# Kernel tuning notes

Measured on AMD Instinct MI355X. Metric: run time of the kernel, lower is better.

Reference implementation:

```python
import jax, jax.numpy as jnp
import numpy as np

B, N, S, D, H, ITERS = 32, 4096, 24, 256, 4, 3
DH = D // H
SCALE = DH ** -0.5
EPS = 1e-8
LN_EPS = 1e-5


def _ln(x, g, b):
    m = x.mean(-1, keepdims=True)
    v = ((x - m) ** 2).mean(-1, keepdims=True)
    return (x - m) * jax.lax.rsqrt(v + LN_EPS) * g + b


def setup_inputs() -> dict:
    key = jax.random.key(0)
    ks = jax.random.split(key, 20)
    xav = lambda k, fi, fo: jax.random.uniform(k, (fi, fo), jnp.float32, -1.0, 1.0) * np.sqrt(6.0 / (fi + fo))
    u = lambda k, shp, fan: jax.random.uniform(k, shp, jnp.float32, -1.0, 1.0) / np.sqrt(fan)
    return {
        "extracted_features": jax.random.normal(ks[0], (B, N, D), jnp.float32),
        "conditioning": jax.random.normal(ks[1], (B, S, D), jnp.float32),
        "pos_ln_g": jnp.ones((D,), jnp.float32),
        "pos_ln_b": jnp.zeros((D,), jnp.float32),
        "pos_w1": xav(ks[2], D, D),
        "pos_b1": jnp.zeros((D,), jnp.float32),
        "pos_w2": xav(ks[3], D, D),
        "pos_b2": jnp.zeros((D,), jnp.float32),
        "in_ln_g": jnp.ones((D,), jnp.float32),
        "in_ln_b": jnp.zeros((D,), jnp.float32),
        "slot_ln_g": jnp.ones((D,), jnp.float32),
        "slot_ln_b": jnp.zeros((D,), jnp.float32),
        "Wq": u(ks[4], (D, D), D),
        "Wk": u(ks[5], (D, D), D),
        "Wv": u(ks[6], (D, D), D),
        "gru_wi": u(ks[7], (D, 3 * D), D),  # x @ gru_wi, torch weight_ih.T
        "gru_wh": u(ks[8], (D, 3 * D), D),
        "gru_bi": u(ks[9], (3 * D,), D),
        "gru_bh": u(ks[10], (3 * D,), D),
    }


def reference(extracted_features, conditioning, pos_ln_g, pos_ln_b, pos_w1, pos_b1,
              pos_w2, pos_b2, in_ln_g, in_ln_b, slot_ln_g, slot_ln_b,
              Wq, Wk, Wv, gru_wi, gru_wh, gru_bi, gru_bh):
    b, n, _ = extracted_features.shape
    s = conditioning.shape[1]
    # positional embedding MLP: LN -> Linear -> ReLU -> Linear
    feats = _ln(extracted_features, pos_ln_g, pos_ln_b)
    feats = jax.nn.relu(feats @ pos_w1 + pos_b1) @ pos_w2 + pos_b2
    # slot attention input norm + k/v projections
    inp = _ln(feats, in_ln_g, in_ln_b)
    k = (inp @ Wk).reshape(b, n, H, DH)
    v = (inp @ Wv).reshape(b, n, H, DH)

    slots = conditioning
    attn_before = None
    for _ in range(ITERS):
        slots_prev = slots
        sn = _ln(slots, slot_ln_g, slot_ln_b)
        q = (sn @ Wq).reshape(b, s, H, DH)
        dots = jnp.einsum('bihd,bjhd->bihj', q, k) * SCALE  # [b,s,H,n]
        # softmax over flattened (slot, head) axis per input token
        attn = jax.nn.softmax(dots.reshape(b, s * H, n), axis=1).reshape(b, s, H, n)
        attn_before = attn
        attn_r = (attn + EPS)
        attn_r = attn_r / attn_r.sum(-1, keepdims=True)
        updates = jnp.einsum('bjhd,bihj->bihd', v, attn_r).reshape(b * s, D)
        # GRUCell update
        h = slots_prev.reshape(b * s, D)
        gi = updates @ gru_wi + gru_bi
        gh = h @ gru_wh + gru_bh
        ir, iz, inn = jnp.split(gi, 3, axis=-1)
        hr, hz, hn = jnp.split(gh, 3, axis=-1)
        r = jax.nn.sigmoid(ir + hr)
        z = jax.nn.sigmoid(iz + hz)
        nn_ = jnp.tanh(inn + r * hn)
        slots = ((1.0 - z) * nn_ + z * h).reshape(b, s, D)

    return slots, attn_before.mean(axis=2)
```

## Files before the change

kernel.cpp:

```cpp
#include <hip/hip_runtime.h>
#include <hip/hip_bf16.h>
#include <stdint.h>

typedef __hip_bfloat16 bf16;
typedef __attribute__((ext_vector_type(8))) short short8;
typedef __attribute__((ext_vector_type(4))) float floatx4;

#define DEV __device__ __forceinline__

DEV float bf2f(bf16 v) { return __bfloat162float(v); }
DEV bf16 f2b(float f) { return __float2bfloat16(f); }
DEV unsigned short f2bu(float f) {
  bf16 h = __float2bfloat16(f);
  union { bf16 h; unsigned short u; } c; c.h = h; return c.u;
}
DEV bool is_bf16_in(const void* probe) { return ((const unsigned short*)probe)[0] != 0; }


__global__ __launch_bounds__(256) void params_kernel(
    const void* s0, const void* s1, const void* s2, const void* s3, const void* s4,
    const void* s5, const void* s6, const void* s7, const void* s8, const void* s9,
    float* dst)
{
  int idx = blockIdx.x * 256 + threadIdx.x;
  if (idx >= 3584) return;
  bool bf = is_bf16_in(s0);
  const void* srcs[10] = {s0, s1, s2, s3, s4, s5, s6, s7, s8, s9};
  int a, off;
  if (idx < 2048)      { a = idx >> 8; off = idx & 255; }
  else if (idx < 2816) { a = 8; off = idx - 2048; }
  else                 { a = 9; off = idx - 2816; }
  float v = bf ? bf2f(((const bf16*)srcs[a])[off]) : ((const float*)srcs[a])[off];
  dst[idx] = v;
}

__global__ __launch_bounds__(256) void transpose_all_kernel(
    const void* w1, const void* w2, const void* wq, const void* wk, const void* wv,
    const void* gwi, const void* gwh,
    bf16* d1, bf16* d2, bf16* dq, bf16* dk, bf16* dv, bf16* dgi, bf16* dgh,
    const void* probe)
{
  int idx = blockIdx.x * 256 + threadIdx.x;
  if (idx >= 720896) return;
  bool bf = is_bf16_in(probe);
  const void* src; bf16* dst; int C, off;
  if (idx < 327680) {
    int wsel = idx >> 16; off = idx & 65535; C = 256;
    const void* S[5] = {w1, w2, wq, wk, wv};
    bf16* D[5] = {d1, d2, dq, dk, dv};
    src = S[wsel]; dst = D[wsel];
  } else {
    int j = idx - 327680; int wsel = j / 196608; off = j - wsel * 196608; C = 768;
    src = wsel ? gwh : gwi; dst = wsel ? dgh : dgi;
  }
  int r = off / C, c = off - r * C;
  bf16 v = bf ? ((const bf16*)src)[off] : f2b(((const float*)src)[off]);
  dst[(size_t)c * 256 + r] = v;
}

__global__ __launch_bounds__(256) void init_slots_kernel(
    const void* __restrict__ cond, float* __restrict__ sF, bf16* __restrict__ sB,
    const void* probe)
{
  int idx = blockIdx.x * 256 + threadIdx.x;
  bool bf = is_bf16_in(probe);
  float v = bf ? bf2f(((const bf16*)cond)[idx]) : ((const float*)cond)[idx];
  sF[idx] = v;
  sB[idx] = f2b(v);
}

template<bool OUT_BF16, bool RELU, bool HAS_BIAS>
DEV void gemm_body(const bf16* __restrict__ A, const bf16* __restrict__ Bt,
                   const float* __restrict__ bias, void* __restrict__ C,
                   int M, int N, int K, int bx, int by, short* As, short* Bs)
{
  const int tid = threadIdx.x;
  const int lane = tid & 63;
  const int wave = tid >> 6;
  const int wr = wave >> 1, wc = wave & 1;
  const int m16 = lane & 15, quad = lane >> 4;
  const long m0 = (long)by * 128, n0 = (long)bx * 128;

  floatx4 acc[4][4];
#pragma unroll
  for (int i = 0; i < 4; i++)
#pragma unroll
    for (int j = 0; j < 4; j++) acc[i][j] = {0.f, 0.f, 0.f, 0.f};

  const int srow = tid >> 3;
  const int scol = (tid & 7) * 8;

  for (int kb = 0; kb < K; kb += 64) {
#pragma unroll
    for (int p = 0; p < 4; p++) {
      int row = srow + p * 32;
      uint4 av = *(const uint4*)(A + (m0 + row) * (long)K + kb + scol);
      *(uint4*)(&As[row * 72 + scol]) = av;
      uint4 bv = *(const uint4*)(Bt + (n0 + row) * (long)K + kb + scol);
      *(uint4*)(&Bs[row * 72 + scol]) = bv;
    }
    __syncthreads();
#pragma unroll
    for (int ks = 0; ks < 2; ks++) {
      short8 af[4], bfr[4];
#pragma unroll
      for (int t = 0; t < 4; t++) {
        af[t]  = *(const short8*)(&As[(wr * 64 + t * 16 + m16) * 72 + ks * 32 + quad * 8]);
        bfr[t] = *(const short8*)(&Bs[(wc * 64 + t * 16 + m16) * 72 + ks * 32 + quad * 8]);
      }
#pragma unroll
      for (int mt = 0; mt < 4; mt++)
#pragma unroll
        for (int nt = 0; nt < 4; nt++)
          acc[mt][nt] = __builtin_amdgcn_mfma_f32_16x16x32_bf16(af[mt], bfr[nt], acc[mt][nt], 0, 0, 0);
    }
    __syncthreads();
  }

#pragma unroll
  for (int mt = 0; mt < 4; mt++) {
#pragma unroll
    for (int nt = 0; nt < 4; nt++) {
      long col = n0 + wc * 64 + nt * 16 + m16;
      float bb = HAS_BIAS ? bias[col] : 0.f;
#pragma unroll
      for (int r = 0; r < 4; r++) {
        long row = m0 + wr * 64 + mt * 16 + quad * 4 + r;
        float v = acc[mt][nt][r] + bb;
        if (RELU) v = fmaxf(v, 0.f);
        if (OUT_BF16) ((bf16*)C)[row * N + col] = f2b(v);
        else          ((float*)C)[row * N + col] = v;
      }
    }
  }
}

__global__ __launch_bounds__(256) void gru2_kernel(
    const bf16* __restrict__ updB, const bf16* __restrict__ sB,
    const bf16* __restrict__ gwit, const bf16* __restrict__ gwht,
    const float* __restrict__ par, float* __restrict__ gi, float* __restrict__ gh)
{
  __shared__ short As[128 * 72];
  __shared__ short Bs[128 * 72];
  if (blockIdx.z == 0)
    gemm_body<false, false, true>(updB, gwit, par + 2048, gi, 768, 768, 256,
                                  blockIdx.x, blockIdx.y, As, Bs);
  else
    gemm_body<false, false, true>(sB, gwht, par + 2816, gh, 768, 768, 256,
                                  blockIdx.x, blockIdx.y, As, Bs);
}


DEV void pa_loadB(uint4 r[4], const bf16* __restrict__ W, int sk, int tid)
{
#pragma unroll
  for (int p = 0; p < 4; p++) {
    int idx = p * 512 + tid;
    int n = idx >> 3, k8 = idx & 7;
    r[p] = *(const uint4*)(W + (size_t)n * 256 + sk * 64 + ((k8 ^ (n & 7)) << 3));
  }
}
DEV void pa_writeB(short* BsBuf, const uint4 r[4], int tid)
{
#pragma unroll
  for (int p = 0; p < 4; p++) {
    int idx = p * 512 + tid;
    int n = idx >> 3, k8 = idx & 7;
    *(uint4*)(&BsBuf[n * 64 + (k8 << 3)]) = r[p];
  }
}

DEV void pa_slice(const short* At, const short* BsBuf, int sk,
                  int wr, int wc, int m16, int quad, floatx4 acc[4][4])
{
#pragma unroll
  for (int ks = 0; ks < 2; ks++) {
    short8 af[4], bfr[4];
#pragma unroll
    for (int t = 0; t < 4; t++) {
      int row = wr * 64 + t * 16 + m16;
      af[t] = *(const short8*)(&At[row * 256 + ((sk * 64 + ks * 32 + quad * 8) ^ ((row & 7) << 3))]);
      int n = wc * 64 + t * 16 + m16;
      bfr[t] = *(const short8*)(&BsBuf[n * 64 + ((ks * 32 + quad * 8) ^ ((n & 7) << 3))]);
    }
#pragma unroll
    for (int mt = 0; mt < 4; mt++)
#pragma unroll
      for (int nt = 0; nt < 4; nt++)
        acc[mt][nt] = __builtin_amdgcn_mfma_f32_16x16x32_bf16(af[mt], bfr[nt], acc[mt][nt], 0, 0, 0);
  }
}

DEV void pa_gemm(const short* At, short* Bs, const bf16* __restrict__ W,
                 int tid, int wr, int wc, int m16, int quad, floatx4 acc[4][4])
{
  uint4 r[4];
  pa_loadB(r, W, 0, tid);
  pa_writeB(Bs, r, tid);
  __syncthreads();
#pragma unroll
  for (int s = 0; s < 4; s++) {
    if (s < 3) pa_loadB(r, W, s + 1, tid);
    pa_slice(At, Bs + (s & 1) * 16384, s, wr, wc, m16, quad, acc);
    if (s < 3) pa_writeB(Bs + ((s + 1) & 1) * 16384, r, tid);
    __syncthreads();
  }
}

DEV void pa_ln_inplace(short* At, const float* __restrict__ par, int goff,
                       int wave, int lane)
{
  float4 gv = *(const float4*)(par + goff + lane * 4);
  float4 bv = *(const float4*)(par + goff + 256 + lane * 4);
#pragma unroll
  for (int i = 0; i < 16; i++) {
    int row = wave * 16 + i;
    int ci = (lane * 4) ^ ((row & 7) << 3);
    uint2 u = *(const uint2*)(&At[row * 256 + ci]);
    float v[4];
    v[0] = __uint_as_float((u.x & 0xffffu) << 16);
    v[1] = __uint_as_float(u.x & 0xffff0000u);
    v[2] = __uint_as_float((u.y & 0xffffu) << 16);
    v[3] = __uint_as_float(u.y & 0xffff0000u);
    float s = v[0] + v[1] + v[2] + v[3];
    float sq = v[0] * v[0] + v[1] * v[1] + v[2] * v[2] + v[3] * v[3];
#pragma unroll
    for (int off = 32; off > 0; off >>= 1) { s += __shfl_xor(s, off); sq += __shfl_xor(sq, off); }
    float mn = s * (1.f / 256.f);
    float rs = rsqrtf(sq * (1.f / 256.f) - mn * mn + 1e-5f);
    union { unsigned short us[4]; uint2 u; } pk;
    pk.us[0] = f2bu((v[0] - mn) * rs * gv.x + bv.x);
    pk.us[1] = f2bu((v[1] - mn) * rs * gv.y + bv.y);
    pk.us[2] = f2bu((v[2] - mn) * rs * gv.z + bv.z);
    pk.us[3] = f2bu((v[3] - mn) * rs * gv.w + bv.w);
    *(uint2*)(&At[row * 256 + ci]) = pk.u;
  }
}

__global__ __launch_bounds__(512, 2) void phasea_kernel(
    const void* __restrict__ x,
    const bf16* __restrict__ w1t, const bf16* __restrict__ w2t,
    const bf16* __restrict__ wkt, const bf16* __restrict__ wvt,
    const float* __restrict__ par,
    bf16* __restrict__ kbuf, bf16* __restrict__ vT, const void* probe)
{
  __shared__ short At[128 * 256];
  __shared__ short Bs[2 * 16384];
  const int tid = threadIdx.x;
  const int lane = tid & 63;
  const int wave = tid >> 6;
  const int wr = wave >> 2, wc = wave & 3;
  const int m16 = lane & 15, quad = lane >> 4;
  const long m0 = (long)blockIdx.x * 128;
  const bool bfin = is_bf16_in(probe);

  {
    float4 gv = *(const float4*)(par + lane * 4);
    float4 bv = *(const float4*)(par + 256 + lane * 4);
#pragma unroll
    for (int i = 0; i < 16; i++) {
      int row = wave * 16 + i;
      float v[4];
      if (bfin) {
        uint2 u = *(const uint2*)((const bf16*)x + (m0 + row) * 256 + lane * 4);
        v[0] = __uint_as_float((u.x & 0xffffu) << 16);
        v[1] = __uint_as_float(u.x & 0xffff0000u);
        v[2] = __uint_as_float((u.y & 0xffffu) << 16);
        v[3] = __uint_as_float(u.y & 0xffff0000u);
      } else {
        float4 f = *(const float4*)((const float*)x + (m0 + row) * 256 + lane * 4);
        v[0] = f.x; v[1] = f.y; v[2] = f.z; v[3] = f.w;
      }
      float s = v[0] + v[1] + v[2] + v[3];
      float sq = v[0] * v[0] + v[1] * v[1] + v[2] * v[2] + v[3] * v[3];
#pragma unroll
      for (int off = 32; off > 0; off >>= 1) { s += __shfl_xor(s, off); sq += __shfl_xor(sq, off); }
      float mn = s * (1.f / 256.f);
      float rs = rsqrtf(sq * (1.f / 256.f) - mn * mn + 1e-5f);
      union { unsigned short us[4]; uint2 u; } pk;
      pk.us[0] = f2bu((v[0] - mn) * rs * gv.x + bv.x);
      pk.us[1] = f2bu((v[1] - mn) * rs * gv.y + bv.y);
      pk.us[2] = f2bu((v[2] - mn) * rs * gv.z + bv.z);
      pk.us[3] = f2bu((v[3] - mn) * rs * gv.w + bv.w);
      *(uint2*)(&At[row * 256 + ((lane * 4) ^ ((row & 7) << 3))]) = pk.u;
    }
  }

  floatx4 acc[4][4];

#pragma unroll
  for (int i = 0; i < 4; i++)
#pragma unroll
    for (int j = 0; j < 4; j++) acc[i][j] = {0.f, 0.f, 0.f, 0.f};
  pa_gemm(At, Bs, w1t, tid, wr, wc, m16, quad, acc);
#pragma unroll
  for (int mt = 0; mt < 4; mt++)
#pragma unroll
    for (int nt = 0; nt < 4; nt++) {
      int col = wc * 64 + nt * 16 + m16;
      float bb = par[512 + col];
#pragma unroll
      for (int r = 0; r < 4; r++) {
        int row = wr * 64 + mt * 16 + quad * 4 + r;
        At[row * 256 + (col ^ ((row & 7) << 3))] = (short)f2bu(fmaxf(acc[mt][nt][r] + bb, 0.f));
      }
    }
  __syncthreads();

#pragma unroll
  for (int i = 0; i < 4; i++)
#pragma unroll
    for (int j = 0; j < 4; j++) acc[i][j] = {0.f, 0.f, 0.f, 0.f};
  pa_gemm(At, Bs, w2t, tid, wr, wc, m16, quad, acc);
#pragma unroll
  for (int mt = 0; mt < 4; mt++)
#pragma unroll
    for (int nt = 0; nt < 4; nt++) {
      int col = wc * 64 + nt * 16 + m16;
      float bb = par[768 + col];
#pragma unroll
      for (int r = 0; r < 4; r++) {
        int row = wr * 64 + mt * 16 + quad * 4 + r;
        At[row * 256 + (col ^ ((row & 7) << 3))] = (short)f2bu(acc[mt][nt][r] + bb);
      }
    }
  __syncthreads();

  pa_ln_inplace(At, par, 1024, wave, lane);
  __syncthreads();

  floatx4 acc4[4][4];
#pragma unroll
  for (int i = 0; i < 4; i++)
#pragma unroll
    for (int j = 0; j < 4; j++) { acc[i][j] = {0.f, 0.f, 0.f, 0.f}; acc4[i][j] = {0.f, 0.f, 0.f, 0.f}; }
  pa_gemm(At, Bs, wkt, tid, wr, wc, m16, quad, acc);
  pa_gemm(At, Bs, wvt, tid, wr, wc, m16, quad, acc4);

#pragma unroll
  for (int mt = 0; mt < 4; mt++)
#pragma unroll
    for (int nt = 0; nt < 4; nt++) {
      int tokb = wr * 64 + mt * 16 + quad * 4;
      int d = wc * 64 + nt * 16 + m16;
#pragma unroll
      for (int r = 0; r < 4; r++) {
        int tok = tokb + r;
        At[tok * 256 + (d ^ ((tok & 7) << 3))] = (short)f2bu(acc[mt][nt][r]);
      }
      union { unsigned short us[4]; uint2 u; } pk;
#pragma unroll
      for (int r = 0; r < 4; r++) pk.us[r] = f2bu(acc4[mt][nt][r]);
      *(uint2*)(&Bs[d * 128 + (tokb ^ ((d & 15) << 3))]) = pk.u;
    }
  __syncthreads();

#pragma unroll
  for (int rr = 0; rr < 8; rr++) {
    int idx = rr * 512 + tid;
    int tok = idx >> 5, dg = (idx & 31) * 8;
    uint4 kv = *(const uint4*)(&At[tok * 256 + (dg ^ ((tok & 7) << 3))]);
    *(uint4*)(kbuf + (m0 + tok) * 256 + dg) = kv;
    int d = idx >> 4, tg = (idx & 15) * 8;
    uint4 vv = *(const uint4*)(&Bs[d * 128 + (tg ^ ((d & 15) << 3))]);
    *(uint4*)(vT + (size_t)d * 131072 + m0 + tg) = vv;
  }
}

__global__ __launch_bounds__(256) void lnq_kernel(
    const float* __restrict__ sF, const bf16* __restrict__ wqt,
    const float* __restrict__ par, bf16* __restrict__ qp)
{
  __shared__ short As[32 * 264];
  const int tid = threadIdx.x;
  const int lane = tid & 63;
  const int wave = tid >> 6;
  const int m16 = lane & 15, quad = lane >> 4;
  const int b = blockIdx.x;

  for (int i = tid; i < 8 * 264; i += 256) As[24 * 264 + i] = 0;

  float4 gv = *(const float4*)(par + 1536 + lane * 4);
  float4 bv = *(const float4*)(par + 1792 + lane * 4);
#pragma unroll
  for (int i = 0; i < 6; i++) {
    int row = wave * 6 + i;
    float4 f = *(const float4*)(sF + ((size_t)(b * 24 + row)) * 256 + lane * 4);
    float v[4] = {f.x, f.y, f.z, f.w};
    float s = v[0] + v[1] + v[2] + v[3];
    float sq = v[0] * v[0] + v[1] * v[1] + v[2] * v[2] + v[3] * v[3];
#pragma unroll
    for (int off = 32; off > 0; off >>= 1) { s += __shfl_xor(s, off); sq += __shfl_xor(sq, off); }
    float mn = s * (1.f / 256.f);
    float rs = rsqrtf(sq * (1.f / 256.f) - mn * mn + 1e-5f);
    union { unsigned short us[4]; uint2 u; } pk;
    pk.us[0] = f2bu((v[0] - mn) * rs * gv.x + bv.x);
    pk.us[1] = f2bu((v[1] - mn) * rs * gv.y + bv.y);
    pk.us[2] = f2bu((v[2] - mn) * rs * gv.z + bv.z);
    pk.us[3] = f2bu((v[3] - mn) * rs * gv.w + bv.w);
    *(uint2*)(&As[row * 264 + lane * 4]) = pk.u;
  }
  __syncthreads();

  floatx4 acc[2][4];
#pragma unroll
  for (int i = 0; i < 2; i++)
#pragma unroll
    for (int j = 0; j < 4; j++) acc[i][j] = {0.f, 0.f, 0.f, 0.f};
#pragma unroll
  for (int ks = 0; ks < 8; ks++) {
    short8 af[2], bfr[4];
#pragma unroll
    for (int mt = 0; mt < 2; mt++)
      af[mt] = *(const short8*)(&As[(mt * 16 + m16) * 264 + ks * 32 + quad * 8]);
#pragma unroll
    for (int nt = 0; nt < 4; nt++)
      bfr[nt] = *(const short8*)(wqt + (size_t)(wave * 64 + nt * 16 + m16) * 256 + ks * 32 + quad * 8);
#pragma unroll
    for (int mt = 0; mt < 2; mt++)
#pragma unroll
      for (int nt = 0; nt < 4; nt++)
        acc[mt][nt] = __builtin_amdgcn_mfma_f32_16x16x32_bf16(af[mt], bfr[nt], acc[mt][nt], 0, 0, 0);
  }

  bf16* qpb = qp + (size_t)(b * 4 + wave) * 2048;
#pragma unroll
  for (int mt = 0; mt < 2; mt++)
#pragma unroll
    for (int nt = 0; nt < 4; nt++)
#pragma unroll
      for (int r = 0; r < 4; r++) {
        int m = mt * 16 + quad * 4 + r;
        qpb[m * 64 + nt * 16 + m16] = f2b(acc[mt][nt][r] * 0.125f);
      }
}

template<bool LAST>
__global__ __launch_bounds__(256) void attn_iter_kernel(
    const bf16* __restrict__ qp, const bf16* __restrict__ kbuf,
    const bf16* __restrict__ vT, float* __restrict__ pupd,
    void* __restrict__ out, const void* __restrict__ probe)
{
  const int js = blockIdx.x;
  const int b  = blockIdx.y;
  const int h  = threadIdx.x >> 6;
  const int lane = threadIdx.x & 63;
  const int m16 = lane & 15, quad = lane >> 4;

  __shared__ unsigned short att[4 * 24 * 136];
  __shared__ float red1[4 * 132];
  __shared__ float red2[4 * 132];

  short8 qf[2][2];
  const bf16* qpb = qp + (size_t)(b * 4 + h) * 2048;
#pragma unroll
  for (int mt = 0; mt < 2; mt++)
#pragma unroll
    for (int ks = 0; ks < 2; ks++)
      qf[mt][ks] = *(const short8*)(qpb + (mt * 16 + m16) * 64 + ks * 32 + quad * 8);

  const bool mt1_valid = (quad < 2);
  int arow1 = 16 + m16; if (arow1 > 23) arow1 = 23;

  floatx4 uacc[2][4];
#pragma unroll
  for (int i = 0; i < 2; i++)
#pragma unroll
    for (int j = 0; j < 4; j++) uacc[i][j] = {0.f, 0.f, 0.f, 0.f};
  float wsum[2][4] = {{0.f, 0.f, 0.f, 0.f}, {0.f, 0.f, 0.f, 0.f}};

  for (int hh = 0; hh < 2; hh++) {
    const int j0 = js * 256 + hh * 128;

    floatx4 dacc[2][8];
#pragma unroll
    for (int i = 0; i < 2; i++)
#pragma unroll
      for (int j = 0; j < 8; j++) dacc[i][j] = {0.f, 0.f, 0.f, 0.f};

    const bf16* kb = kbuf + ((size_t)b * 4096 + j0) * 256 + h * 64;
#pragma unroll
    for (int ks = 0; ks < 2; ks++)
#pragma unroll
      for (int nt = 0; nt < 8; nt++) {
        short8 bfr = *(const short8*)(kb + (size_t)(nt * 16 + m16) * 256 + ks * 32 + quad * 8);
        dacc[0][nt] = __builtin_amdgcn_mfma_f32_16x16x32_bf16(qf[0][ks], bfr, dacc[0][nt], 0, 0, 0);
        dacc[1][nt] = __builtin_amdgcn_mfma_f32_16x16x32_bf16(qf[1][ks], bfr, dacc[1][nt], 0, 0, 0);
      }

    float cmax[8];
#pragma unroll
    for (int nt = 0; nt < 8; nt++) {
      float m = fmaxf(fmaxf(dacc[0][nt][0], dacc[0][nt][1]), fmaxf(dacc[0][nt][2], dacc[0][nt][3]));
      if (mt1_valid)
        m = fmaxf(m, fmaxf(fmaxf(dacc[1][nt][0], dacc[1][nt][1]), fmaxf(dacc[1][nt][2], dacc[1][nt][3])));
      m = fmaxf(m, __shfl_xor(m, 16));
      m = fmaxf(m, __shfl_xor(m, 32));
      cmax[nt] = m;
    }
    if (quad == 0) {
#pragma unroll
      for (int nt = 0; nt < 8; nt++) red1[h * 132 + nt * 16 + m16] = cmax[nt];
    }
    __syncthreads();

    float csum[8];
#pragma unroll
    for (int nt = 0; nt < 8; nt++) {
      int c = nt * 16 + m16;
      float g = fmaxf(fmaxf(red1[c], red1[132 + c]), fmaxf(red1[264 + c], red1[396 + c]));
      float s = 0.f;
#pragma unroll
      for (int r = 0; r < 4; r++) {
        float e = __expf(dacc[0][nt][r] - g);
        dacc[0][nt][r] = e; s += e;
      }
#pragma unroll
      for (int r = 0; r < 4; r++) {
        float e = mt1_valid ? __expf(dacc[1][nt][r] - g) : 0.f;
        dacc[1][nt][r] = e; s += e;
      }
      s += __shfl_xor(s, 16);
      s += __shfl_xor(s, 32);
      csum[nt] = s;
    }
    if (quad == 0) {
#pragma unroll
      for (int nt = 0; nt < 8; nt++) red2[h * 132 + nt * 16 + m16] = csum[nt];
    }
    __syncthreads();

#pragma unroll
    for (int nt = 0; nt < 8; nt++) {
      int c = nt * 16 + m16;
      float inv = 1.f / (red2[c] + red2[132 + c] + red2[264 + c] + red2[396 + c]);
#pragma unroll
      for (int r = 0; r < 4; r++) {
        float a = dacc[0][nt][r] * inv + 1e-8f;
        att[h * 3264 + (quad * 4 + r) * 136 + c] = f2bu(a);
        wsum[0][r] += a;
      }
      if (mt1_valid) {
#pragma unroll
        for (int r = 0; r < 4; r++) {
          float a = dacc[1][nt][r] * inv + 1e-8f;
          att[h * 3264 + (16 + quad * 4 + r) * 136 + c] = f2bu(a);
          wsum[1][r] += a;
        }
      }
    }
    __syncthreads();

    const bf16* vb0 = vT + (size_t)b * 4096 + j0;
#pragma unroll
    for (int ks = 0; ks < 4; ks++) {
      short8 a0 = *(const short8*)(&att[h * 3264 + m16 * 136 + ks * 32 + quad * 8]);
      short8 a1 = *(const short8*)(&att[h * 3264 + arow1 * 136 + ks * 32 + quad * 8]);
#pragma unroll
      for (int nt = 0; nt < 4; nt++) {
        short8 bfr = *(const short8*)(vb0 + (size_t)(h * 64 + nt * 16 + m16) * 131072 + ks * 32 + quad * 8);
        uacc[0][nt] = __builtin_amdgcn_mfma_f32_16x16x32_bf16(a0, bfr, uacc[0][nt], 0, 0, 0);
        uacc[1][nt] = __builtin_amdgcn_mfma_f32_16x16x32_bf16(a1, bfr, uacc[1][nt], 0, 0, 0);
      }
    }

    if (LAST) {
      const bool bfo = is_bf16_in(probe);
      int c = threadIdx.x & 127;
      int half = threadIdx.x >> 7;
#pragma unroll
      for (int i0 = 0; i0 < 12; i0++) {
        int i = half * 12 + i0;
        float s = bf2f(__ushort_as_bfloat16(att[i * 136 + c]))
                + bf2f(__ushort_as_bfloat16(att[3264 + i * 136 + c]))
                + bf2f(__ushort_as_bfloat16(att[6528 + i * 136 + c]))
                + bf2f(__ushort_as_bfloat16(att[9792 + i * 136 + c]));
        size_t oidx = ((size_t)(b * 24 + i)) * 4096 + j0 + c;
        if (bfo) ((bf16*)out)[196608 + oidx] = f2b(0.25f * s);
        else     ((float*)out)[196608 + oidx] = 0.25f * s;
      }
    }
    __syncthreads();
  }

  float* dst = pupd + ((size_t)((b * 4 + h) * 16 + js)) * 1920;
#pragma unroll
  for (int mt = 0; mt < 2; mt++)
#pragma unroll
    for (int r = 0; r < 4; r++) {
      float w = wsum[mt][r];
      w += __shfl_xor(w, 1); w += __shfl_xor(w, 2);
      w += __shfl_xor(w, 4); w += __shfl_xor(w, 8);
      wsum[mt][r] = w;
    }
  if (m16 == 0) {
#pragma unroll
    for (int mt = 0; mt < 2; mt++)
#pragma unroll
      for (int r = 0; r < 4; r++) {
        int row = mt * 16 + quad * 4 + r;
        if (row < 24) dst[row * 80 + 64] = wsum[mt][r];
      }
  }
#pragma unroll
  for (int mt = 0; mt < 2; mt++)
#pragma unroll
    for (int nt = 0; nt < 4; nt++)
#pragma unroll
      for (int r = 0; r < 4; r++) {
        int row = mt * 16 + quad * 4 + r;
        if (row < 24) dst[row * 80 + nt * 16 + m16] = uacc[mt][nt][r];
      }
}

__global__ __launch_bounds__(256) void upd_final_kernel(
    const float* __restrict__ pupd, bf16* __restrict__ updB)
{
  int bh = blockIdx.x; int b = bh >> 2, h = bh & 3;
  int idx = blockIdx.y * 256 + threadIdx.x;
  int i = idx >> 6, d = idx & 63;
  const float* base = pupd + (size_t)bh * 16 * 1920 + i * 80;
  float v = 0.f, w = 0.f;
#pragma unroll
  for (int p = 0; p < 16; p++) {
    v += base[p * 1920 + d];
    w += base[p * 1920 + 64];
  }
  updB[((size_t)(b * 24 + i)) * 256 + h * 64 + d] = f2b(v / w);
}

template<bool LAST>
__global__ __launch_bounds__(256) void gru_gate_kernel(
    const float* __restrict__ gi, const float* __restrict__ gh,
    float* __restrict__ sF, bf16* __restrict__ sB,
    void* __restrict__ out, const void* __restrict__ probe)
{
  int row = blockIdx.x, d = threadIdx.x;
  size_t o = (size_t)row * 768;
  float ir = gi[o + d], iz = gi[o + 256 + d], inn = gi[o + 512 + d];
  float hr = gh[o + d], hz = gh[o + 256 + d], hn = gh[o + 512 + d];
  float hv = sF[(size_t)row * 256 + d];
  float r = 1.f / (1.f + __expf(-(ir + hr)));
  float z = 1.f / (1.f + __expf(-(iz + hz)));
  float nn = tanhf(inn + r * hn);
  float sv = (1.f - z) * nn + z * hv;
  sF[(size_t)row * 256 + d] = sv;
  sB[(size_t)row * 256 + d] = f2b(sv);
  if (LAST) {
    if (is_bf16_in(probe)) ((bf16*)out)[(size_t)row * 256 + d] = f2b(sv);
    else                   ((float*)out)[(size_t)row * 256 + d] = sv;
  }
}

static constexpr size_t SZ_BIG   = (size_t)32 * 4096 * 256 * 2;
static constexpr size_t OFF_BUF1 = 0;
static constexpr size_t OFF_BUF2 = OFF_BUF1 + SZ_BIG;
static constexpr size_t OFF_K    = OFF_BUF2 + SZ_BIG;
static constexpr size_t OFF_V    = OFF_K + SZ_BIG;
static constexpr size_t OFF_Q    = OFF_V + SZ_BIG;
static constexpr size_t OFF_QP   = OFF_Q + (size_t)768 * 256 * 4;
static constexpr size_t OFF_SNB  = OFF_QP + (size_t)32 * 4 * 32 * 64 * 2;
static constexpr size_t OFF_SF   = OFF_SNB + (size_t)768 * 256 * 2;
static constexpr size_t OFF_SB   = OFF_SF + (size_t)768 * 256 * 4;
static constexpr size_t OFF_UPD  = OFF_SB + (size_t)768 * 256 * 2;
static constexpr size_t OFF_GI   = OFF_UPD + (size_t)768 * 256 * 2;
static constexpr size_t OFF_GH   = OFF_GI + (size_t)768 * 768 * 4;
static constexpr size_t OFF_PUPD = OFF_GH + (size_t)768 * 768 * 4;
static constexpr size_t OFF_W1T  = OFF_PUPD + (size_t)128 * 32 * 1920 * 4;
static constexpr size_t OFF_W2T  = OFF_W1T + (size_t)256 * 256 * 2;
static constexpr size_t OFF_WQT  = OFF_W2T + (size_t)256 * 256 * 2;
static constexpr size_t OFF_WKT  = OFF_WQT + (size_t)256 * 256 * 2;
static constexpr size_t OFF_WVT  = OFF_WKT + (size_t)256 * 256 * 2;
static constexpr size_t OFF_GWIT = OFF_WVT + (size_t)256 * 256 * 2;
static constexpr size_t OFF_GWHT = OFF_GWIT + (size_t)256 * 768 * 2;
static constexpr size_t OFF_PAR  = OFF_GWHT + (size_t)256 * 768 * 2;
static constexpr size_t OFF_FLAG = OFF_PAR + (size_t)3584 * 4;
static constexpr size_t WS_NEED  = OFF_FLAG + 256;

extern "C" void kernel_launch(void* const* d_in, const int* in_sizes, int n_in,
                              void* d_out, int out_size, void* d_ws, size_t ws_size,
                              hipStream_t stream) {
  (void)in_sizes; (void)n_in; (void)out_size;
  if (ws_size < WS_NEED) return;

  const void* x         = d_in[0];
  const void* cond      = d_in[1];
  const void* pos_ln_g  = d_in[2];
  const void* pos_ln_b  = d_in[3];
  const void* pos_w1    = d_in[4];
  const void* pos_b1    = d_in[5];
  const void* pos_w2    = d_in[6];
  const void* pos_b2    = d_in[7];
  const void* in_ln_g   = d_in[8];
  const void* in_ln_b   = d_in[9];
  const void* slot_ln_g = d_in[10];
  const void* slot_ln_b = d_in[11];
  const void* Wq        = d_in[12];
  const void* Wk        = d_in[13];
  const void* Wv        = d_in[14];
  const void* gru_wi    = d_in[15];
  const void* gru_wh    = d_in[16];
  const void* gru_bi    = d_in[17];
  const void* gru_bh    = d_in[18];

  char* ws = (char*)d_ws;
  bf16*  kbuf  = (bf16*)(ws + OFF_K);
  bf16*  vT    = (bf16*)(ws + OFF_V);
  bf16*  qp    = (bf16*)(ws + OFF_QP);
  float* sF    = (float*)(ws + OFF_SF);
  bf16*  sB    = (bf16*)(ws + OFF_SB);
  bf16*  updB  = (bf16*)(ws + OFF_UPD);
  float* gi    = (float*)(ws + OFF_GI);
  float* gh    = (float*)(ws + OFF_GH);
  float* pupd  = (float*)(ws + OFF_PUPD);
  bf16*  w1t   = (bf16*)(ws + OFF_W1T);
  bf16*  w2t   = (bf16*)(ws + OFF_W2T);
  bf16*  wqt   = (bf16*)(ws + OFF_WQT);
  bf16*  wkt   = (bf16*)(ws + OFF_WKT);
  bf16*  wvt   = (bf16*)(ws + OFF_WVT);
  bf16*  gwit  = (bf16*)(ws + OFF_GWIT);
  bf16*  gwht  = (bf16*)(ws + OFF_GWHT);
  float* par   = (float*)(ws + OFF_PAR);

  const void* probe = pos_ln_g;

  params_kernel<<<14, 256, 0, stream>>>(pos_ln_g, pos_ln_b, pos_b1, pos_b2,
                                        in_ln_g, in_ln_b, slot_ln_g, slot_ln_b,
                                        gru_bi, gru_bh, par);
  transpose_all_kernel<<<2816, 256, 0, stream>>>(pos_w1, pos_w2, Wq, Wk, Wv, gru_wi, gru_wh,
                                                 w1t, w2t, wqt, wkt, wvt, gwit, gwht, probe);
  init_slots_kernel<<<768, 256, 0, stream>>>(cond, sF, sB, probe);

  phasea_kernel<<<1024, 512, 0, stream>>>(x, w1t, w2t, wkt, wvt, par, kbuf, vT, probe);

  for (int it = 0; it < 3; it++) {
    lnq_kernel<<<32, 256, 0, stream>>>(sF, wqt, par, qp);
    if (it == 2)
      attn_iter_kernel<true><<<dim3(16, 32), 256, 0, stream>>>(qp, kbuf, vT, pupd, d_out, probe);
    else
      attn_iter_kernel<false><<<dim3(16, 32), 256, 0, stream>>>(qp, kbuf, vT, pupd, d_out, probe);
    upd_final_kernel<<<dim3(128, 6), 256, 0, stream>>>(pupd, updB);
    gru2_kernel<<<dim3(6, 6, 2), 256, 0, stream>>>(updB, sB, gwit, gwht, par, gi, gh);
    if (it == 2)
      gru_gate_kernel<true><<<768, 256, 0, stream>>>(gi, gh, sF, sB, d_out, probe);
    else
      gru_gate_kernel<false><<<768, 256, 0, stream>>>(gi, gh, sF, sB, d_out, probe);
  }
}
```

Baseline: 586.0 us.

## Halve phase-A row tile to 64 tokens with 4 waves and K-step 32

The fused LN+MLP+K/V projection kernel now processes 64 tokens per block with 256 threads instead of 128 tokens with 512. Each wave owns a 64-column slice across all rows, and the weight tile is streamed in 32-wide K slices through a double-buffered register/LDS pipeline with a new XOR swizzle. LDS per block drops by half, which may let more blocks fit per CU and doubles the grid to 2048 blocks. The cost is that weight tiles are reloaded twice as often per token, and there are twice as many barriers per GEMM.

```diff
diff --git a/kernel.cpp b/kernel.cpp
--- a/kernel.cpp
+++ b/kernel.cpp
@@ -155,54 +155,57 @@
 {
 #pragma unroll
   for (int p = 0; p < 4; p++) {
-    int idx = p * 512 + tid;
-    int n = idx >> 3, k8 = idx & 7;
-    r[p] = *(const uint4*)(W + (size_t)n * 256 + sk * 64 + ((k8 ^ (n & 7)) << 3));
+    int idx = p * 256 + tid;
+    int n = idx >> 2, phys = idx & 3;
+    int l = phys ^ ((n >> 1) & 3);
+    r[p] = *(const uint4*)(W + (size_t)n * 256 + sk * 32 + l * 8);
   }
 }
 DEV void pa_writeB(short* BsBuf, const uint4 r[4], int tid)
 {
 #pragma unroll
   for (int p = 0; p < 4; p++) {
-    int idx = p * 512 + tid;
-    int n = idx >> 3, k8 = idx & 7;
-    *(uint4*)(&BsBuf[n * 64 + (k8 << 3)]) = r[p];
+    int idx = p * 256 + tid;
+    int n = idx >> 2, phys = idx & 3;
+    *(uint4*)(&BsBuf[n * 32 + phys * 8]) = r[p];
   }
 }
 
 DEV void pa_slice(const short* At, const short* BsBuf, int sk,
-                  int wr, int wc, int m16, int quad, floatx4 acc[4][4])
-{
-#pragma unroll
-  for (int ks = 0; ks < 2; ks++) {
-    short8 af[4], bfr[4];
-#pragma unroll
-    for (int t = 0; t < 4; t++) {
-      int row = wr * 64 + t * 16 + m16;
-      af[t] = *(const short8*)(&At[row * 256 + ((sk * 64 + ks * 32 + quad * 8) ^ ((row & 7) << 3))]);
-      int n = wc * 64 + t * 16 + m16;
-      bfr[t] = *(const short8*)(&BsBuf[n * 64 + ((ks * 32 + quad * 8) ^ ((n & 7) << 3))]);
-    }
-#pragma unroll
-    for (int mt = 0; mt < 4; mt++)
-#pragma unroll
-      for (int nt = 0; nt < 4; nt++)
-        acc[mt][nt] = __builtin_amdgcn_mfma_f32_16x16x32_bf16(af[mt], bfr[nt], acc[mt][nt], 0, 0, 0);
-  }
+                  int wave, int m16, int quad, floatx4 acc[4][4])
+{
+  short8 af[4], bfr[4];
+#pragma unroll
+  for (int t = 0; t < 4; t++) {
+    int row = t * 16 + m16;
+    af[t] = *(const short8*)(&At[row * 256 + ((sk * 32 + quad * 8) ^ ((row & 7) << 3))]);
+    int n = wave * 64 + t * 16 + m16;
+    int phys = quad ^ ((n >> 1) & 3);
+    bfr[t] = *(const short8*)(&BsBuf[n * 32 + phys * 8]);
+  }
+#pragma unroll
+  for (int mt = 0; mt < 4; mt++)
+#pragma unroll
+    for (int nt = 0; nt < 4; nt++)
+      acc[mt][nt] = __builtin_amdgcn_mfma_f32_16x16x32_bf16(af[mt], bfr[nt], acc[mt][nt], 0, 0, 0);
 }
 
 DEV void pa_gemm(const short* At, short* Bs, const bf16* __restrict__ W,
-                 int tid, int wr, int wc, int m16, int quad, floatx4 acc[4][4])
-{
-  uint4 r[4];
-  pa_loadB(r, W, 0, tid);
-  pa_writeB(Bs, r, tid);
+                 int tid, int wave, int m16, int quad, floatx4 acc[4][4])
+{
+  uint4 ra[4], rb[4];
+  pa_loadB(ra, W, 0, tid);
+  pa_loadB(rb, W, 1, tid);
+  pa_writeB(Bs, ra, tid);
   __syncthreads();
 #pragma unroll
-  for (int s = 0; s < 4; s++) {
-    if (s < 3) pa_loadB(r, W, s + 1, tid);
-    pa_slice(At, Bs + (s & 1) * 16384, s, wr, wc, m16, quad, acc);
-    if (s < 3) pa_writeB(Bs + ((s + 1) & 1) * 16384, r, tid);
+  for (int s = 0; s < 8; s++) {
+    if (s < 7) pa_writeB(Bs + ((s + 1) & 1) * 8192, ((s + 1) & 1) ? rb : ra, tid);
+    if (s < 6) {
+      if (s & 1) pa_loadB(rb, W, s + 2, tid);
+      else       pa_loadB(ra, W, s + 2, tid);
+    }
+    pa_slice(At, Bs + (s & 1) * 8192, s, wave, m16, quad, acc);
     __syncthreads();
   }
 }
@@ -237,21 +240,20 @@
   }
 }
 
-__global__ __launch_bounds__(512, 2) void phasea_kernel(
+__global__ __launch_bounds__(256, 2) void phasea_kernel(
     const void* __restrict__ x,
     const bf16* __restrict__ w1t, const bf16* __restrict__ w2t,
     const bf16* __restrict__ wkt, const bf16* __restrict__ wvt,
     const float* __restrict__ par,
     bf16* __restrict__ kbuf, bf16* __restrict__ vT, const void* probe)
 {
-  __shared__ short At[128 * 256];
-  __shared__ short Bs[2 * 16384];
+  __shared__ short At[64 * 256];
+  __shared__ short Bs[2 * 8192];
   const int tid = threadIdx.x;
   const int lane = tid & 63;
   const int wave = tid >> 6;
-  const int wr = wave >> 2, wc = wave & 3;
   const int m16 = lane & 15, quad = lane >> 4;
-  const long m0 = (long)blockIdx.x * 128;
+  const long m0 = (long)blockIdx.x * 64;
   const bool bfin = is_bf16_in(probe);
 
   {
@@ -285,6 +287,7 @@
       *(uint2*)(&At[row * 256 + ((lane * 4) ^ ((row & 7) << 3))]) = pk.u;
     }
   }
+  __syncthreads();
 
   floatx4 acc[4][4];
 
@@ -292,16 +295,16 @@
   for (int i = 0; i < 4; i++)
 #pragma unroll
     for (int j = 0; j < 4; j++) acc[i][j] = {0.f, 0.f, 0.f, 0.f};
-  pa_gemm(At, Bs, w1t, tid, wr, wc, m16, quad, acc);
+  pa_gemm(At, Bs, w1t, tid, wave, m16, quad, acc);
 #pragma unroll
   for (int mt = 0; mt < 4; mt++)
 #pragma unroll
     for (int nt = 0; nt < 4; nt++) {
-      int col = wc * 64 + nt * 16 + m16;
+      int col = wave * 64 + nt * 16 + m16;
       float bb = par[512 + col];
 #pragma unroll
       for (int r = 0; r < 4; r++) {
-        int row = wr * 64 + mt * 16 + quad * 4 + r;
+        int row = mt * 16 + quad * 4 + r;
         At[row * 256 + (col ^ ((row & 7) << 3))] = (short)f2bu(fmaxf(acc[mt][nt][r] + bb, 0.f));
       }
     }
@@ -311,16 +314,16 @@
   for (int i = 0; i < 4; i++)
 #pragma unroll
     for (int j = 0; j < 4; j++) acc[i][j] = {0.f, 0.f, 0.f, 0.f};
-  pa_gemm(At, Bs, w2t, tid, wr, wc, m16, quad, acc);
+  pa_gemm(At, Bs, w2t, tid, wave, m16, quad, acc);
 #pragma unroll
   for (int mt = 0; mt < 4; mt++)
 #pragma unroll
     for (int nt = 0; nt < 4; nt++) {
-      int col = wc * 64 + nt * 16 + m16;
+      int col = wave * 64 + nt * 16 + m16;
       float bb = par[768 + col];
 #pragma unroll
       for (int r = 0; r < 4; r++) {
-        int row = wr * 64 + mt * 16 + quad * 4 + r;
+        int row = mt * 16 + quad * 4 + r;
         At[row * 256 + (col ^ ((row & 7) << 3))] = (short)f2bu(acc[mt][nt][r] + bb);
       }
     }
@@ -334,15 +337,15 @@
   for (int i = 0; i < 4; i++)
 #pragma unroll
     for (int j = 0; j < 4; j++) { acc[i][j] = {0.f, 0.f, 0.f, 0.f}; acc4[i][j] = {0.f, 0.f, 0.f, 0.f}; }
-  pa_gemm(At, Bs, wkt, tid, wr, wc, m16, quad, acc);
-  pa_gemm(At, Bs, wvt, tid, wr, wc, m16, quad, acc4);
+  pa_gemm(At, Bs, wkt, tid, wave, m16, quad, acc);
+  pa_gemm(At, Bs, wvt, tid, wave, m16, quad, acc4);
 
 #pragma unroll
   for (int mt = 0; mt < 4; mt++)
 #pragma unroll
     for (int nt = 0; nt < 4; nt++) {
-      int tokb = wr * 64 + mt * 16 + quad * 4;
-      int d = wc * 64 + nt * 16 + m16;
+      int d = wave * 64 + nt * 16 + m16;
+      int tokb = mt * 16 + quad * 4;
 #pragma unroll
       for (int r = 0; r < 4; r++) {
         int tok = tokb + r;
@@ -351,19 +354,20 @@
       union { unsigned short us[4]; uint2 u; } pk;
 #pragma unroll
       for (int r = 0; r < 4; r++) pk.us[r] = f2bu(acc4[mt][nt][r]);
-      *(uint2*)(&Bs[d * 128 + (tokb ^ ((d & 15) << 3))]) = pk.u;
+      int phys = (tokb >> 3) ^ (d & 7);
+      *(uint2*)(&Bs[d * 64 + phys * 8 + (tokb & 7)]) = pk.u;
     }
   __syncthreads();
 
 #pragma unroll
   for (int rr = 0; rr < 8; rr++) {
-    int idx = rr * 512 + tid;
+    int idx = rr * 256 + tid;
     int tok = idx >> 5, dg = (idx & 31) * 8;
     uint4 kv = *(const uint4*)(&At[tok * 256 + (dg ^ ((tok & 7) << 3))]);
     *(uint4*)(kbuf + (m0 + tok) * 256 + dg) = kv;
-    int d = idx >> 4, tg = (idx & 15) * 8;
-    uint4 vv = *(const uint4*)(&Bs[d * 128 + (tg ^ ((d & 15) << 3))]);
-    *(uint4*)(vT + (size_t)d * 131072 + m0 + tg) = vv;
+    int d = idx >> 3, s8 = idx & 7;
+    uint4 vv = *(const uint4*)(&Bs[d * 64 + ((s8 ^ (d & 7)) * 8)]);
+    *(uint4*)(vT + (size_t)d * 131072 + m0 + s8 * 8) = vv;
   }
 }
 
@@ -731,7 +735,7 @@
                                                  w1t, w2t, wqt, wkt, wvt, gwit, gwht, probe);
   init_slots_kernel<<<768, 256, 0, stream>>>(cond, sF, sB, probe);
 
-  phasea_kernel<<<1024, 512, 0, stream>>>(x, w1t, w2t, wkt, wvt, par, kbuf, vT, probe);
+  phasea_kernel<<<2048, 256, 0, stream>>>(x, w1t, w2t, wkt, wvt, par, kbuf, vT, probe);
 
   for (int it = 0; it < 3; it++) {
     lnq_kernel<<<32, 256, 0, stream>>>(sF, wqt, par, qp);
```

New measurement: 778.6 us. +32.9%, slower.
